# Kernel tuning notes

Measured on AMD Instinct MI355X. Metric: run time of the kernel, lower is better.

The kernel has to match this reference:

```python
import jax, jax.numpy as jnp
import numpy as np

N, E, F_IN, F_E, HID, HEADS = 20000, 320000, 256, 32, 128, 4
NEG_SLOPE = 0.2  # PyG GATConv default negative_slope


def _segment_softmax(logits, seg, num_segments):
    # logits: [E, H] softmax over edges sharing the same destination node
    m = jax.ops.segment_max(logits, seg, num_segments=num_segments)
    m = jnp.where(jnp.isfinite(m), m, 0.0)
    e = jnp.exp(logits - m[seg])
    s = jax.ops.segment_sum(e, seg, num_segments=num_segments)
    return e / s[seg]


def _gat_layer(x, edge_attr, src, dst, W, We, a_src, a_dst, a_edge, bias, num_nodes):
    H, C = a_src.shape
    h = (x @ W).reshape(-1, H, C)            # [N, H, C]
    he = (edge_attr @ We).reshape(-1, H, C)  # [E, H, C]
    alpha = (h * a_src).sum(-1)[src] + (h * a_dst).sum(-1)[dst] + (he * a_edge).sum(-1)
    alpha = jax.nn.leaky_relu(alpha, NEG_SLOPE)          # [E, H]
    alpha = _segment_softmax(alpha, dst, num_nodes)
    out = jax.ops.segment_sum(h[src] * alpha[..., None], dst, num_segments=num_nodes)
    return out.reshape(num_nodes, H * C) + bias


def setup_inputs() -> dict:
    key = jax.random.key(0)
    ks = jax.random.split(key, 20)
    s1 = 1.0 / np.sqrt(F_IN)
    s2 = 1.0 / np.sqrt(HID * HEADS)
    se = 1.0 / np.sqrt(F_E)
    sh = 1.0 / np.sqrt(HID)
    return {
        "x": jax.random.normal(ks[0], (N, F_IN), jnp.float32),
        "edge_index": jax.random.randint(ks[1], (2, E), 0, N),
        "edge_attr": jax.random.normal(ks[2], (E, F_E), jnp.float32),
        # GAT layer 1: in=F_IN, heads=HEADS, out=HID, concat=True
        "W1": jax.random.normal(ks[3], (F_IN, HEADS * HID), jnp.float32) * s1,
        "We1": jax.random.normal(ks[4], (F_E, HEADS * HID), jnp.float32) * se,
        "as1": jax.random.normal(ks[5], (HEADS, HID), jnp.float32) * sh,
        "ad1": jax.random.normal(ks[6], (HEADS, HID), jnp.float32) * sh,
        "ae1": jax.random.normal(ks[7], (HEADS, HID), jnp.float32) * sh,
        "b1": jnp.zeros((HEADS * HID,), jnp.float32),
        # GAT layer 2: in=HEADS*HID, heads=1, out=HID
        "W2": jax.random.normal(ks[8], (HEADS * HID, HID), jnp.float32) * s2,
        "We2": jax.random.normal(ks[9], (F_E, HID), jnp.float32) * se,
        "as2": jax.random.normal(ks[10], (1, HID), jnp.float32) * sh,
        "ad2": jax.random.normal(ks[11], (1, HID), jnp.float32) * sh,
        "ae2": jax.random.normal(ks[12], (1, HID), jnp.float32) * sh,
        "b2": jnp.zeros((HID,), jnp.float32),
        # projection head: Linear(HID,HID) -> PReLU -> Linear(HID,HID)
        "P1": jax.random.normal(ks[13], (HID, HID), jnp.float32) * sh,
        "pb1": jnp.zeros((HID,), jnp.float32),
        "prelu_a": jnp.float32(0.25),
        "P2": jax.random.normal(ks[14], (HID, HID), jnp.float32) * sh,
        "pb2": jnp.zeros((HID,), jnp.float32),
    }


def reference(x, edge_index, edge_attr, W1, We1, as1, ad1, ae1, b1,
              W2, We2, as2, ad2, ae2, b2, P1, pb1, prelu_a, P2, pb2):
    # eval mode: edge dropout / feature dropout are no-ops
    ei = jnp.concatenate([edge_index, edge_index[::-1]], axis=1)  # add reversed edges
    ea = jnp.concatenate([edge_attr, edge_attr], axis=0)
    src, dst = ei[0], ei[1]
    n = x.shape[0]
    h = jax.nn.elu(_gat_layer(x, ea, src, dst, W1, We1, as1, ad1, ae1, b1, n))
    h = jax.nn.elu(_gat_layer(h, ea, src, dst, W2, We2, as2, ad2, ae2, b2, n))
    z = h @ P1 + pb1
    z = jnp.where(z > 0, z, prelu_a * z)  # PReLU (single shared parameter)
    h_proj = z @ P2 + pb2
    g = jax.nn.sigmoid(h_proj.mean(axis=0))
    return h_proj, g
```

## Files before the change

### kernel.cpp

```cpp
#include <hip/hip_runtime.h>
#include <hip/hip_bf16.h>


#define NN    20000
#define EE    320000
#define E2    640000
#define FIN   256
#define FE    32
#define HIDD  128
#define NHEAD 4
#define HH    512
#define CAP   160
#define AW    132

typedef unsigned short ushort_t;
typedef short frag8 __attribute__((ext_vector_type(8)));
typedef float f32x4 __attribute__((ext_vector_type(4)));

__device__ inline ushort_t f2bf(float f){
  unsigned x = __float_as_uint(f);
  unsigned r = (x + 0x7fffu + ((x>>16)&1u)) >> 16;
  return (ushort_t)r;
}
__device__ inline float bf2f(ushort_t u){ return __uint_as_float(((unsigned)u)<<16); }
__device__ inline float lo_of(unsigned v){ return __uint_as_float(v<<16); }
__device__ inline float hi_of(unsigned v){ return __uint_as_float(v & 0xffff0000u); }

__global__ void prep(const int* __restrict__ ei, int* __restrict__ cnt,
                     const float* __restrict__ x, ushort_t* __restrict__ xb,
                     const float* __restrict__ W1, ushort_t* __restrict__ W1t,
                     const float* __restrict__ W2, ushort_t* __restrict__ W2t,
                     const float* __restrict__ P1, ushort_t* __restrict__ P1th, ushort_t* __restrict__ P1tl,
                     const float* __restrict__ P2, ushort_t* __restrict__ P2th, ushort_t* __restrict__ P2tl,
                     const float* __restrict__ We1, const float* __restrict__ ae1,
                     const float* __restrict__ We2, const float* __restrict__ ae2,
                     float* __restrict__ v1, float* __restrict__ v2){
  int b = blockIdx.x, tid = threadIdx.x;
  if(b < 2500){
    int e = b*256 + tid;
    int dst = (e < EE) ? ei[EE + e] : ei[e - EE];
    atomicAdd(&cnt[dst], 1);
  } else if(b < 7500){
    int i = (b-2500)*256 + tid;
    float4 v = ((const float4*)x)[i];
    ushort4 o; o.x=f2bf(v.x); o.y=f2bf(v.y); o.z=f2bf(v.z); o.w=f2bf(v.w);
    ((ushort4*)xb)[i] = o;
  } else if(b < 8012){
    int idx = (b-7500)*256 + tid;
    int k = idx>>9, n = idx&511;
    W1t[n*FIN + k] = f2bf(W1[idx]);
  } else if(b < 8268){
    int idx = (b-8012)*256 + tid;
    int k = idx>>7, n = idx&127;
    W2t[n*HH + k] = f2bf(W2[idx]);
  } else if(b < 8332){
    int idx = (b-8268)*256 + tid;
    int k = idx>>7, n = idx&127;
    float v = P1[idx];
    ushort_t h = f2bf(v);
    P1th[n*HIDD + k] = h;
    P1tl[n*HIDD + k] = f2bf(v - bf2f(h));
  } else if(b < 8396){
    int idx = (b-8332)*256 + tid;
    int k = idx>>7, n = idx&127;
    float v = P2[idx];
    ushort_t h = f2bf(v);
    P2th[n*HIDD + k] = h;
    P2tl[n*HIDD + k] = f2bf(v - bf2f(h));
  } else {
    if(tid < FE*NHEAD){
      int f = tid>>2, h = tid&3;
      float s = 0.f;
      for(int c=0;c<HIDD;c++) s += We1[f*HH + h*HIDD + c] * ae1[h*HIDD + c];
      v1[f*4+h] = s;
    } else if(tid < FE*NHEAD + FE){
      int f = tid - FE*NHEAD;
      float s = 0.f;
      for(int c=0;c<HIDD;c++) s += We2[f*HIDD + c] * ae2[c];
      v2[f] = s;
    }
  }
}

__global__ void scan_k(const int* __restrict__ cnt, int* __restrict__ rowptr){
  __shared__ int sums[1024];
  int tid = threadIdx.x;
  const int per = (NN + 1023)/1024;
  int base = tid*per;
  int s = 0;
  for(int i=0;i<per;i++){ int idx=base+i; if(idx<NN) s += cnt[idx]; }
  sums[tid] = s; __syncthreads();
  for(int off=1; off<1024; off<<=1){
    int v = (tid>=off)? sums[tid-off] : 0;
    __syncthreads();
    sums[tid] += v;
    __syncthreads();
  }
  int run = (tid==0)? 0 : sums[tid-1];
  for(int i=0;i<per;i++){
    int idx = base+i;
    if(idx<=NN) rowptr[idx] = run;
    if(idx<NN)  run += cnt[idx];
  }
}

__global__ __launch_bounds__(256) void csr_gemm1(
    const int* __restrict__ ei, const float* __restrict__ ea,
    const float* __restrict__ v1, const float* __restrict__ v2,
    const int* __restrict__ rowptr, int* __restrict__ fcnt,
    int* __restrict__ csrc, float* __restrict__ cae1, float* __restrict__ cae2,
    const ushort_t* __restrict__ A, const ushort_t* __restrict__ Bt,
    ushort_t* __restrict__ C, int M,
    const float* __restrict__ as1, const float* __restrict__ ad1,
    float* __restrict__ s1n, float* __restrict__ d1n){
  __shared__ ushort_t As[128*32];
  __shared__ ushort_t Bs[128*32];
  __shared__ float sred[2][128], dred[2][128];
  __shared__ float sv1[FE*NHEAD];
  __shared__ float sv2[FE];
  int tid = threadIdx.x;
  int b = blockIdx.x;
  if(b < 1250){
    if(tid < FE*NHEAD) sv1[tid] = v1[tid];
    if(tid < FE)       sv2[tid] = v2[tid];
    __syncthreads();
    int e = b*256 + tid;
    int a = ei[e], bb = ei[EE+e];
    const float4* er4 = (const float4*)(ea + (long)e*FE);
    float a0=0,a1=0,a2=0,a3=0,ab=0;
    #pragma unroll
    for(int f4=0; f4<FE/4; f4++){
      float4 t = er4[f4];
      float tv[4] = {t.x, t.y, t.z, t.w};
      #pragma unroll
      for(int c=0;c<4;c++){
        int f = f4*4+c;
        float t1 = tv[c];
        a0 += t1*sv1[f*4+0]; a1 += t1*sv1[f*4+1]; a2 += t1*sv1[f*4+2]; a3 += t1*sv1[f*4+3];
        ab += t1*sv2[f];
      }
    }
    float4 c4; c4.x=a0; c4.y=a1; c4.z=a2; c4.w=a3;
    int pos = rowptr[bb] + atomicAdd(&fcnt[bb], 1);
    csrc[pos] = a;
    *(float4*)(cae1 + (size_t)pos*4) = c4;
    cae2[pos] = ab;
    pos = rowptr[a] + atomicAdd(&fcnt[a], 1);
    csrc[pos] = bb;
    *(float4*)(cae1 + (size_t)pos*4) = c4;
    cae2[pos] = ab;
    return;
  }
  int g = b - 1250;
  int head = g & 3;
  int m0 = (g>>2)*128, n0 = head*128;
  int w = tid>>6, lane = tid&63;
  int qr = (w>>1)*64, qc = (w&1)*64;
  int lrow = lane&15, koff = (lane>>4)*8;
  f32x4 acc[4][4] = {};
  for(int k0=0; k0<FIN; k0+=32){
    #pragma unroll
    for(int rep=0;rep<2;rep++){
      int segid = tid + rep*256;
      int row = segid>>2, off = (segid&3)*8;
      int gr = m0 + row;
      int4 va = (gr<M) ? *(const int4*)(A + (long)gr*FIN + k0 + off) : int4{0,0,0,0};
      *(int4*)&As[row*32 + off] = va;
      int4 vb = *(const int4*)(Bt + (long)(n0+row)*FIN + k0 + off);
      *(int4*)&Bs[row*32 + off] = vb;
    }
    __syncthreads();
    frag8 af[4], bfr[4];
    #pragma unroll
    for(int i=0;i<4;i++) af[i]  = *(const frag8*)&As[(qr + i*16 + lrow)*32 + koff];
    #pragma unroll
    for(int j=0;j<4;j++) bfr[j] = *(const frag8*)&Bs[(qc + j*16 + lrow)*32 + koff];
    #pragma unroll
    for(int i=0;i<4;i++)
      #pragma unroll
      for(int j=0;j<4;j++)
        acc[i][j] = __builtin_amdgcn_mfma_f32_16x16x32_bf16(af[i], bfr[j], acc[i][j], 0,0,0);
    __syncthreads();
  }
  #pragma unroll
  for(int i=0;i<4;i++)
    #pragma unroll
    for(int j=0;j<4;j++)
      #pragma unroll
      for(int r=0;r<4;r++){
        int row = m0 + qr + i*16 + (lane>>4)*4 + r;
        int col = n0 + qc + j*16 + (lane&15);
        if(row<M) C[(long)row*HH + col] = f2bf(acc[i][j][r]);
      }
  float a_s[4], a_d[4];
  #pragma unroll
  for(int j=0;j<4;j++){
    a_s[j] = as1[head*HIDD + qc + j*16 + (lane&15)];
    a_d[j] = ad1[head*HIDD + qc + j*16 + (lane&15)];
  }
  #pragma unroll
  for(int i=0;i<4;i++)
    #pragma unroll
    for(int r=0;r<4;r++){
      float sp = acc[i][0][r]*a_s[0] + acc[i][1][r]*a_s[1] + acc[i][2][r]*a_s[2] + acc[i][3][r]*a_s[3];
      float dp = acc[i][0][r]*a_d[0] + acc[i][1][r]*a_d[1] + acc[i][2][r]*a_d[2] + acc[i][3][r]*a_d[3];
      #pragma unroll
      for(int o=1;o<=8;o<<=1){ sp += __shfl_xor(sp,o,64); dp += __shfl_xor(dp,o,64); }
      if((lane&15)==0){
        int rl = qr + i*16 + (lane>>4)*4 + r;
        sred[w&1][rl] = sp;
        dred[w&1][rl] = dp;
      }
    }
  __syncthreads();
  if(tid < 128){
    int gr = m0 + tid;
    if(gr < M){
      s1n[gr*4 + head] = sred[0][tid] + sred[1][tid];
      d1n[gr*4 + head] = dred[0][tid] + dred[1][tid];
    }
  }
}

__global__ __launch_bounds__(256) void gemm64_attn(const ushort_t* __restrict__ A, const ushort_t* __restrict__ Bt,
                                                   ushort_t* __restrict__ C, int M,
                                                   const float* __restrict__ as2, const float* __restrict__ ad2,
                                                   float* __restrict__ s2n, float* __restrict__ d2n){
  __shared__ ushort_t As[64*32];
  __shared__ ushort_t Bs[128*32];
  __shared__ float sred[4][64], dred[4][64];
  int tid = threadIdx.x;
  int m0 = blockIdx.y*64;
  int w = tid>>6, lane = tid&63;
  int qc = w*32;
  int lrow = lane&15, koff = (lane>>4)*8;
  f32x4 acc[4][2] = {};
  for(int k0=0; k0<HH; k0+=32){
    {
      int row = tid>>2, off = (tid&3)*8;
      int gr = m0 + row;
      int4 va = (gr<M) ? *(const int4*)(A + (long)gr*HH + k0 + off) : int4{0,0,0,0};
      *(int4*)&As[row*32 + off] = va;
    }
    #pragma unroll
    for(int rep=0;rep<2;rep++){
      int segid = tid + rep*256;
      int row = segid>>2, off = (segid&3)*8;
      int4 vb = *(const int4*)(Bt + (long)row*HH + k0 + off);
      *(int4*)&Bs[row*32 + off] = vb;
    }
    __syncthreads();
    frag8 af[4], bfr[2];
    #pragma unroll
    for(int i=0;i<4;i++) af[i]  = *(const frag8*)&As[(i*16 + lrow)*32 + koff];
    #pragma unroll
    for(int j=0;j<2;j++) bfr[j] = *(const frag8*)&Bs[(qc + j*16 + lrow)*32 + koff];
    #pragma unroll
    for(int i=0;i<4;i++)
      #pragma unroll
      for(int j=0;j<2;j++)
        acc[i][j] = __builtin_amdgcn_mfma_f32_16x16x32_bf16(af[i], bfr[j], acc[i][j], 0,0,0);
    __syncthreads();
  }
  #pragma unroll
  for(int i=0;i<4;i++)
    #pragma unroll
    for(int j=0;j<2;j++)
      #pragma unroll
      for(int r=0;r<4;r++){
        int row = m0 + i*16 + (lane>>4)*4 + r;
        int col = qc + j*16 + (lane&15);
        if(row<M) C[(long)row*HIDD + col] = f2bf(acc[i][j][r]);
      }
  float a_s[2], a_d[2];
  #pragma unroll
  for(int j=0;j<2;j++){
    a_s[j] = as2[qc + j*16 + (lane&15)];
    a_d[j] = ad2[qc + j*16 + (lane&15)];
  }
  #pragma unroll
  for(int i=0;i<4;i++)
    #pragma unroll
    for(int r=0;r<4;r++){
      float sp = acc[i][0][r]*a_s[0] + acc[i][1][r]*a_s[1];
      float dp = acc[i][0][r]*a_d[0] + acc[i][1][r]*a_d[1];
      #pragma unroll
      for(int o=1;o<=8;o<<=1){ sp += __shfl_xor(sp,o,64); dp += __shfl_xor(dp,o,64); }
      if((lane&15)==0){
        int rl = i*16 + (lane>>4)*4 + r;
        sred[w][rl] = sp;
        dred[w][rl] = dp;
      }
    }
  __syncthreads();
  if(tid < 64){
    int gr = m0 + tid;
    if(gr < M){
      s2n[gr] = sred[0][tid]+sred[1][tid]+sred[2][tid]+sred[3][tid];
      d2n[gr] = dred[0][tid]+dred[1][tid]+dred[2][tid]+dred[3][tid];
    }
  }
}

__global__ __launch_bounds__(256) void agg1(const ushort_t* __restrict__ h1b, const int* __restrict__ rowptr,
                     const int* __restrict__ csrc,
                     const float* __restrict__ s1n, const float* __restrict__ d1n,
                     const float* __restrict__ cae1,
                     const float* __restrict__ b1, ushort_t* __restrict__ out1b){
  __shared__ float stlog[4][CAP*4];
  __shared__ int   sidx[4][CAP];
  int tid = threadIdx.x;
  int wv = tid>>6, lane = tid&63;
  int n = blockIdx.x*4 + wv;
  int beg = rowptr[n], end = rowptr[n+1];
  int deg = end - beg;
  int h12 = lane&3;
  float dh = d1n[n*4 + h12];
  float m = -1e30f, ss = 0.f;
  for(int base=beg; base<end; base+=16){
    int e = base + (lane>>2);
    if(e<end){
      int s = csrc[e];
      float t = s1n[s*4 + h12] + dh + cae1[e*4 + h12];
      t = t>0.f? t : 0.2f*t;
      int j = e - beg;
      if(j < CAP){
        stlog[wv][j*4 + h12] = t;
        if(h12==0) sidx[wv][j] = s;
      }
      float nm = fmaxf(m, t);
      ss = ss*__expf(m-nm) + __expf(t-nm);
      m = nm;
    }
  }
  #pragma unroll
  for(int o=4;o<=32;o<<=1){
    float mo = __shfl_xor(m, o, 64), so = __shfl_xor(ss, o, 64);
    float nm = fmaxf(m, mo);
    ss = ss*__expf(m-nm) + so*__expf(mo-nm);
    m = nm;
  }
  float inv = ss>0.f ? 1.f/ss : 0.f;
  int hq = lane>>4;
  float mq   = __shfl(m,   hq, 64);
  float invq = __shfl(inv, hq, 64);
  float dhq  = d1n[n*4 + hq];
  int capn = deg < CAP ? deg : CAP;
  float acc[8] = {};
  int j = 0;
  for(; j+3<capn; j+=4){
    int s0 = sidx[wv][j], s1 = sidx[wv][j+1], s2 = sidx[wv][j+2], s3 = sidx[wv][j+3];
    float w0 = __expf(stlog[wv][(j  )*4 + hq] - mq)*invq;
    float w1 = __expf(stlog[wv][(j+1)*4 + hq] - mq)*invq;
    float w2 = __expf(stlog[wv][(j+2)*4 + hq] - mq)*invq;
    float w3 = __expf(stlog[wv][(j+3)*4 + hq] - mq)*invq;
    uint4 v0 = *(const uint4*)(h1b + (long)s0*HH + lane*8);
    uint4 v1 = *(const uint4*)(h1b + (long)s1*HH + lane*8);
    uint4 v2 = *(const uint4*)(h1b + (long)s2*HH + lane*8);
    uint4 v3 = *(const uint4*)(h1b + (long)s3*HH + lane*8);
    acc[0] += w0*lo_of(v0.x) + w1*lo_of(v1.x) + w2*lo_of(v2.x) + w3*lo_of(v3.x);
    acc[1] += w0*hi_of(v0.x) + w1*hi_of(v1.x) + w2*hi_of(v2.x) + w3*hi_of(v3.x);
    acc[2] += w0*lo_of(v0.y) + w1*lo_of(v1.y) + w2*lo_of(v2.y) + w3*lo_of(v3.y);
    acc[3] += w0*hi_of(v0.y) + w1*hi_of(v1.y) + w2*hi_of(v2.y) + w3*hi_of(v3.y);
    acc[4] += w0*lo_of(v0.z) + w1*lo_of(v1.z) + w2*lo_of(v2.z) + w3*lo_of(v3.z);
    acc[5] += w0*hi_of(v0.z) + w1*hi_of(v1.z) + w2*hi_of(v2.z) + w3*hi_of(v3.z);
    acc[6] += w0*lo_of(v0.w) + w1*lo_of(v1.w) + w2*lo_of(v2.w) + w3*lo_of(v3.w);
    acc[7] += w0*hi_of(v0.w) + w1*hi_of(v1.w) + w2*hi_of(v2.w) + w3*hi_of(v3.w);
  }
  for(; j<capn; j++){
    int s0 = sidx[wv][j];
    float w0 = __expf(stlog[wv][j*4 + hq] - mq)*invq;
    uint4 v0 = *(const uint4*)(h1b + (long)s0*HH + lane*8);
    acc[0] += w0*lo_of(v0.x); acc[1] += w0*hi_of(v0.x);
    acc[2] += w0*lo_of(v0.y); acc[3] += w0*hi_of(v0.y);
    acc[4] += w0*lo_of(v0.z); acc[5] += w0*hi_of(v0.z);
    acc[6] += w0*lo_of(v0.w); acc[7] += w0*hi_of(v0.w);
  }
  for(; j<deg; j++){
    int e = beg + j;
    int s0 = csrc[e];
    float t = s1n[s0*4 + hq] + dhq + cae1[e*4 + hq];
    t = t>0.f? t : 0.2f*t;
    float w0 = __expf(t - mq)*invq;
    uint4 v0 = *(const uint4*)(h1b + (long)s0*HH + lane*8);
    acc[0] += w0*lo_of(v0.x); acc[1] += w0*hi_of(v0.x);
    acc[2] += w0*lo_of(v0.y); acc[3] += w0*hi_of(v0.y);
    acc[4] += w0*lo_of(v0.z); acc[5] += w0*hi_of(v0.z);
    acc[6] += w0*lo_of(v0.w); acc[7] += w0*hi_of(v0.w);
  }
  float4 bl = ((const float4*)b1)[lane*2];
  float4 bh = ((const float4*)b1)[lane*2+1];
  float bb[8] = {bl.x,bl.y,bl.z,bl.w,bh.x,bh.y,bh.z,bh.w};
  ushort_t o8[8];
  #pragma unroll
  for(int c=0;c<8;c++){
    float o = acc[c] + bb[c];
    o8[c] = f2bf(o>0.f? o : __expf(o)-1.f);
  }
  uint4 pk;
  pk.x = (unsigned)o8[0] | ((unsigned)o8[1]<<16);
  pk.y = (unsigned)o8[2] | ((unsigned)o8[3]<<16);
  pk.z = (unsigned)o8[4] | ((unsigned)o8[5]<<16);
  pk.w = (unsigned)o8[6] | ((unsigned)o8[7]<<16);
  *(uint4*)(out1b + (long)n*HH + lane*8) = pk;
}

__global__ __launch_bounds__(256) void agg2(const ushort_t* __restrict__ h2b, const int* __restrict__ rowptr,
                     const int* __restrict__ csrc,
                     const float* __restrict__ s2n, const float* __restrict__ d2n,
                     const float* __restrict__ cae2,
                     const float* __restrict__ b2, float* __restrict__ out2){
  __shared__ float stl[4][CAP];
  __shared__ int   sid[4][CAP];
  int tid = threadIdx.x;
  int wv = tid>>6, lane = tid&63;
  int n = blockIdx.x*4 + wv;
  int beg = rowptr[n], end = rowptr[n+1];
  int deg = end - beg;
  float dn = d2n[n];
  float m = -1e30f, ss = 0.f;
  for(int e=beg+lane; e<end; e+=64){
    int s = csrc[e];
    float t = s2n[s] + dn + cae2[e];
    t = t>0.f? t : 0.2f*t;
    int j = e - beg;
    if(j < CAP){ stl[wv][j] = t; sid[wv][j] = s; }
    float nm = fmaxf(m, t);
    ss = ss*__expf(m-nm) + __expf(t-nm);
    m = nm;
  }
  #pragma unroll
  for(int o=1;o<=32;o<<=1){
    float mo = __shfl_xor(m, o, 64), so = __shfl_xor(ss, o, 64);
    float nm = fmaxf(m, mo);
    ss = ss*__expf(m-nm) + so*__expf(mo-nm);
    m = nm;
  }
  float inv = ss>0.f ? 1.f/ss : 0.f;
  int capn = deg < CAP ? deg : CAP;
  float a0=0.f, a1=0.f;
  int j = 0;
  for(; j+3<capn; j+=4){
    int s0 = sid[wv][j], s1 = sid[wv][j+1], s2 = sid[wv][j+2], s3 = sid[wv][j+3];
    float w0 = __expf(stl[wv][j]  -m)*inv;
    float w1 = __expf(stl[wv][j+1]-m)*inv;
    float w2 = __expf(stl[wv][j+2]-m)*inv;
    float w3 = __expf(stl[wv][j+3]-m)*inv;
    unsigned v0 = *(const unsigned*)(h2b + (long)s0*HIDD + 2*lane);
    unsigned v1 = *(const unsigned*)(h2b + (long)s1*HIDD + 2*lane);
    unsigned v2 = *(const unsigned*)(h2b + (long)s2*HIDD + 2*lane);
    unsigned v3 = *(const unsigned*)(h2b + (long)s3*HIDD + 2*lane);
    a0 += w0*lo_of(v0) + w1*lo_of(v1) + w2*lo_of(v2) + w3*lo_of(v3);
    a1 += w0*hi_of(v0) + w1*hi_of(v1) + w2*hi_of(v2) + w3*hi_of(v3);
  }
  for(; j<capn; j++){
    float w0 = __expf(stl[wv][j]-m)*inv;
    unsigned v0 = *(const unsigned*)(h2b + (long)sid[wv][j]*HIDD + 2*lane);
    a0 += w0*lo_of(v0); a1 += w0*hi_of(v0);
  }
  for(; j<deg; j++){
    int e = beg + j;
    int s0 = csrc[e];
    float t = s2n[s0] + dn + cae2[e];
    t = t>0.f? t : 0.2f*t;
    float w0 = __expf(t-m)*inv;
    unsigned v0 = *(const unsigned*)(h2b + (long)s0*HIDD + 2*lane);
    a0 += w0*lo_of(v0); a1 += w0*hi_of(v0);
  }
  float o0 = a0 + b2[2*lane];
  float o1 = a1 + b2[2*lane+1];
  float2 pk;
  pk.x = o0>0.f? o0 : __expf(o0)-1.f;
  pk.y = o1>0.f? o1 : __expf(o1)-1.f;
  *(float2*)(out2 + (long)n*HIDD + 2*lane) = pk;
}

__global__ __launch_bounds__(256) void proj_fused(const float* __restrict__ A,
    const ushort_t* __restrict__ P1th, const ushort_t* __restrict__ P1tl,
    const ushort_t* __restrict__ P2th, const ushort_t* __restrict__ P2tl,
    const float* __restrict__ pb1, const float* __restrict__ pra,
    const float* __restrict__ pb2, float* __restrict__ OUT, int M,
    float* __restrict__ gbuf){
  __shared__ ushort_t Ah[64*AW], Al[64*AW];
  __shared__ ushort_t Bh[128*32], Bl[128*32];
  int tid = threadIdx.x;
  int m0 = blockIdx.x*64;
  int w = tid>>6, lane = tid&63;
  int qc = w*32;
  int lrow = lane&15, koff2 = (lane>>4)*8;
  f32x4 acc[4][2] = {};
  {
    int row = tid>>2, cb = (tid&3)*8;
    int gr = m0 + row;
    for(int c0=0;c0<HIDD;c0+=32){
      float4 u0{0,0,0,0}, u1{0,0,0,0};
      if(gr<M){
        u0 = *(const float4*)(A + (long)gr*HIDD + c0 + cb);
        u1 = *(const float4*)(A + (long)gr*HIDD + c0 + cb + 4);
      }
      float vv[8] = {u0.x,u0.y,u0.z,u0.w,u1.x,u1.y,u1.z,u1.w};
      unsigned ph[4], pl[4];
      #pragma unroll
      for(int c=0;c<4;c++){
        ushort_t h0 = f2bf(vv[2*c]),   l0 = f2bf(vv[2*c]   - bf2f(h0));
        ushort_t h1 = f2bf(vv[2*c+1]), l1 = f2bf(vv[2*c+1] - bf2f(h1));
        ph[c] = (unsigned)h0 | ((unsigned)h1<<16);
        pl[c] = (unsigned)l0 | ((unsigned)l1<<16);
      }
      *(uint4*)&Ah[row*AW + c0 + cb] = *(uint4*)ph;
      *(uint4*)&Al[row*AW + c0 + cb] = *(uint4*)pl;
    }
  }
  __syncthreads();
  for(int k0=0;k0<HIDD;k0+=32){
    #pragma unroll
    for(int rep=0;rep<2;rep++){
      int segid = tid + rep*256;
      int row = segid>>2, off = (segid&3)*8;
      *(int4*)&Bh[row*32 + off] = *(const int4*)(P1th + (long)row*HIDD + k0 + off);
      *(int4*)&Bl[row*32 + off] = *(const int4*)(P1tl + (long)row*HIDD + k0 + off);
    }
    __syncthreads();
    frag8 afh[4], afl[4], bfh[2], bfl[2];
    #pragma unroll
    for(int i=0;i<4;i++){
      afh[i] = *(const frag8*)&Ah[(i*16 + lrow)*AW + k0 + koff2];
      afl[i] = *(const frag8*)&Al[(i*16 + lrow)*AW + k0 + koff2];
    }
    #pragma unroll
    for(int j=0;j<2;j++){
      bfh[j] = *(const frag8*)&Bh[(qc + j*16 + lrow)*32 + koff2];
      bfl[j] = *(const frag8*)&Bl[(qc + j*16 + lrow)*32 + koff2];
    }
    #pragma unroll
    for(int i=0;i<4;i++)
      #pragma unroll
      for(int j=0;j<2;j++){
        acc[i][j] = __builtin_amdgcn_mfma_f32_16x16x32_bf16(afh[i], bfh[j], acc[i][j], 0,0,0);
        acc[i][j] = __builtin_amdgcn_mfma_f32_16x16x32_bf16(afh[i], bfl[j], acc[i][j], 0,0,0);
        acc[i][j] = __builtin_amdgcn_mfma_f32_16x16x32_bf16(afl[i], bfh[j], acc[i][j], 0,0,0);
      }
    __syncthreads();
  }
  float ap = pra[0];
  #pragma unroll
  for(int i=0;i<4;i++)
    #pragma unroll
    for(int j=0;j<2;j++)
      #pragma unroll
      for(int r=0;r<4;r++){
        int row = i*16 + (lane>>4)*4 + r;
        int col = qc + j*16 + (lane&15);
        float v = acc[i][j][r] + pb1[col];
        v = v>0.f? v : ap*v;
        ushort_t h = f2bf(v);
        Ah[row*AW + col] = h;
        Al[row*AW + col] = f2bf(v - bf2f(h));
        acc[i][j][r] = 0.f;
      }
  __syncthreads();
  for(int k0=0;k0<HIDD;k0+=32){
    #pragma unroll
    for(int rep=0;rep<2;rep++){
      int segid = tid + rep*256;
      int row = segid>>2, off = (segid&3)*8;
      *(int4*)&Bh[row*32 + off] = *(const int4*)(P2th + (long)row*HIDD + k0 + off);
      *(int4*)&Bl[row*32 + off] = *(const int4*)(P2tl + (long)row*HIDD + k0 + off);
    }
    __syncthreads();
    frag8 afh[4], afl[4], bfh[2], bfl[2];
    #pragma unroll
    for(int i=0;i<4;i++){
      afh[i] = *(const frag8*)&Ah[(i*16 + lrow)*AW + k0 + koff2];
      afl[i] = *(const frag8*)&Al[(i*16 + lrow)*AW + k0 + koff2];
    }
    #pragma unroll
    for(int j=0;j<2;j++){
      bfh[j] = *(const frag8*)&Bh[(qc + j*16 + lrow)*32 + koff2];
      bfl[j] = *(const frag8*)&Bl[(qc + j*16 + lrow)*32 + koff2];
    }
    #pragma unroll
    for(int i=0;i<4;i++)
      #pragma unroll
      for(int j=0;j<2;j++){
        acc[i][j] = __builtin_amdgcn_mfma_f32_16x16x32_bf16(afh[i], bfh[j], acc[i][j], 0,0,0);
        acc[i][j] = __builtin_amdgcn_mfma_f32_16x16x32_bf16(afh[i], bfl[j], acc[i][j], 0,0,0);
        acc[i][j] = __builtin_amdgcn_mfma_f32_16x16x32_bf16(afl[i], bfh[j], acc[i][j], 0,0,0);
      }
    __syncthreads();
  }
  float cs[2] = {0.f, 0.f};
  #pragma unroll
  for(int i=0;i<4;i++)
    #pragma unroll
    for(int j=0;j<2;j++)
      #pragma unroll
      for(int r=0;r<4;r++){
        int rowg = m0 + i*16 + (lane>>4)*4 + r;
        int col = qc + j*16 + (lane&15);
        if(rowg<M){
          float v = acc[i][j][r] + pb2[col];
          OUT[(long)rowg*HIDD + col] = v;
          cs[j] += v;
        }
      }
  #pragma unroll
  for(int j=0;j<2;j++){
    cs[j] += __shfl_xor(cs[j],16,64);
    cs[j] += __shfl_xor(cs[j],32,64);
    if((lane>>4)==0) atomicAdd(&gbuf[qc + j*16 + (lane&15)], cs[j]);
  }
}

__global__ void sigmoid_g(const float* __restrict__ gbuf, float* __restrict__ gout){
  int c = threadIdx.x;
  float m = gbuf[c] * (1.0f/NN);
  gout[c] = 1.f/(1.f+__expf(-m));
}


extern "C" void kernel_launch(void* const* d_in, const int* in_sizes, int n_in,
                              void* d_out, int out_size, void* d_ws, size_t ws_size,
                              hipStream_t stream){
  const float* x    = (const float*)d_in[0];
  const int*   ei   = (const int*)  d_in[1];
  const float* ea   = (const float*)d_in[2];
  const float* W1   = (const float*)d_in[3];
  const float* We1  = (const float*)d_in[4];
  const float* as1  = (const float*)d_in[5];
  const float* ad1  = (const float*)d_in[6];
  const float* ae1  = (const float*)d_in[7];
  const float* b1   = (const float*)d_in[8];
  const float* W2   = (const float*)d_in[9];
  const float* We2  = (const float*)d_in[10];
  const float* as2  = (const float*)d_in[11];
  const float* ad2  = (const float*)d_in[12];
  const float* ae2  = (const float*)d_in[13];
  const float* b2   = (const float*)d_in[14];
  const float* P1   = (const float*)d_in[15];
  const float* pb1  = (const float*)d_in[16];
  const float* pra  = (const float*)d_in[17];
  const float* P2   = (const float*)d_in[18];
  const float* pb2  = (const float*)d_in[19];
  float* out = (float*)d_out;

  char* wsp = (char*)d_ws;
  size_t off = 0;
  auto alloc = [&](size_t bytes)->char*{
    char* p = wsp + off;
    off += (bytes + 255) & ~(size_t)255;
    return p;
  };
  ushort_t* h1b  = (ushort_t*)alloc(sizeof(ushort_t)*(size_t)NN*HH);
  ushort_t* out1b= (ushort_t*)alloc(sizeof(ushort_t)*(size_t)NN*HH);
  ushort_t* h2b  = (ushort_t*)alloc(sizeof(ushort_t)*(size_t)NN*HIDD);
  float*    out2 = (float*)  alloc(sizeof(float)*(size_t)NN*HIDD);
  ushort_t* xb   = (ushort_t*)alloc(sizeof(ushort_t)*(size_t)NN*FIN);
  ushort_t* W1t  = (ushort_t*)alloc(sizeof(ushort_t)*(size_t)HH*FIN);
  ushort_t* W2t  = (ushort_t*)alloc(sizeof(ushort_t)*(size_t)HIDD*HH);
  ushort_t* P1th = (ushort_t*)alloc(sizeof(ushort_t)*(size_t)HIDD*HIDD);
  ushort_t* P1tl = (ushort_t*)alloc(sizeof(ushort_t)*(size_t)HIDD*HIDD);
  ushort_t* P2th = (ushort_t*)alloc(sizeof(ushort_t)*(size_t)HIDD*HIDD);
  ushort_t* P2tl = (ushort_t*)alloc(sizeof(ushort_t)*(size_t)HIDD*HIDD);
  float* s1n   = (float*)alloc(sizeof(float)*NN*NHEAD);
  float* d1n   = (float*)alloc(sizeof(float)*NN*NHEAD);
  float* s2n   = (float*)alloc(sizeof(float)*NN);
  float* d2n   = (float*)alloc(sizeof(float)*NN);
  float* v1    = (float*)alloc(sizeof(float)*FE*NHEAD);
  float* v2    = (float*)alloc(sizeof(float)*FE);
  float* cae1  = (float*)alloc(sizeof(float)*(size_t)E2*NHEAD);
  float* cae2  = (float*)alloc(sizeof(float)*(size_t)E2);
  int*   rowptr= (int*)  alloc(sizeof(int)*(NN+1));
  int*   csrc  = (int*)  alloc(sizeof(int)*(size_t)E2);
  int*   cnt   = (int*)  alloc(sizeof(int)*NN);
  int*   fcnt  = (int*)  alloc(sizeof(int)*NN);
  float* gbuf  = (float*)alloc(sizeof(float)*HIDD);

  hipMemsetAsync(cnt, 0, 80128 + 80128 + 512, stream);

  prep     <<<8397, 256, 0, stream>>>(ei, cnt, x, xb, W1, W1t, W2, W2t,
                                      P1, P1th, P1tl, P2, P2th, P2tl,
                                      We1, ae1, We2, ae2, v1, v2);
  scan_k   <<<1, 1024, 0, stream>>>(cnt, rowptr);
  csr_gemm1<<<1250 + 628, 256, 0, stream>>>(ei, ea, v1, v2, rowptr, fcnt, csrc, cae1, cae2,
                                            xb, W1t, h1b, NN, as1, ad1, s1n, d1n);
  agg1     <<<NN/4, 256, 0, stream>>>(h1b, rowptr, csrc, s1n, d1n, cae1, b1, out1b);
  gemm64_attn<<<dim3(1, (NN+63)/64), 256, 0, stream>>>(out1b, W2t, h2b, NN, as2, ad2, s2n, d2n);
  agg2     <<<NN/4, 256, 0, stream>>>(h2b, rowptr, csrc, s2n, d2n, cae2, b2, out2);
  proj_fused<<<(NN+63)/64, 256, 0, stream>>>(out2, P1th, P1tl, P2th, P2tl,
                                             pb1, pra, pb2, out, NN, gbuf);
  sigmoid_g<<<1, 128, 0, stream>>>(gbuf, out + (size_t)NN*HIDD);
}
```

Before: 394.8 us.

## Split agg1 nodes across two waves, precompute softmax weights, vectorize scan

Result: faster. 373.4 us (-5.4%).

```diff
diff --git a/kernel.cpp b/kernel.cpp
--- a/kernel.cpp
+++ b/kernel.cpp
@@ -85,23 +85,38 @@
 __global__ void scan_k(const int* __restrict__ cnt, int* __restrict__ rowptr){
   __shared__ int sums[1024];
   int tid = threadIdx.x;
-  const int per = (NN + 1023)/1024;
+  const int per = 20;
   int base = tid*per;
+  int v[20];
+  if(base + per <= NN){
+    #pragma unroll
+    for(int q=0;q<5;q++) *(int4*)&v[q*4] = *(const int4*)&cnt[base + q*4];
+  } else {
+    for(int i=0;i<per;i++) v[i] = (base+i<NN)? cnt[base+i] : 0;
+  }
   int s = 0;
-  for(int i=0;i<per;i++){ int idx=base+i; if(idx<NN) s += cnt[idx]; }
+  #pragma unroll
+  for(int i=0;i<per;i++) s += v[i];
   sums[tid] = s; __syncthreads();
   for(int off=1; off<1024; off<<=1){
-    int v = (tid>=off)? sums[tid-off] : 0;
-    __syncthreads();
-    sums[tid] += v;
+    int t = (tid>=off)? sums[tid-off] : 0;
+    __syncthreads();
+    sums[tid] += t;
     __syncthreads();
   }
   int run = (tid==0)? 0 : sums[tid-1];
-  for(int i=0;i<per;i++){
-    int idx = base+i;
-    if(idx<=NN) rowptr[idx] = run;
-    if(idx<NN)  run += cnt[idx];
-  }
+  int rp[20];
+  #pragma unroll
+  for(int i=0;i<per;i++){ rp[i] = run; run += v[i]; }
+  if(base + per <= NN){
+    #pragma unroll
+    for(int q=0;q<5;q++) *(int4*)&rowptr[base + q*4] = *(const int4*)&rp[q*4];
+  } else {
+    for(int i=0;i<per;i++) if(base+i<=NN) rowptr[base+i] = rp[i];
+  }
+  if(base == NN) rowptr[NN] = rp[0];
+  if(tid == 1023 && base + per == NN) rowptr[NN] = run;
+  if(tid == 1000) rowptr[NN] = rp[0];
 }
 
 __global__ __launch_bounds__(256) void csr_gemm1(
@@ -307,17 +322,20 @@
                      const float* __restrict__ s1n, const float* __restrict__ d1n,
                      const float* __restrict__ cae1,
                      const float* __restrict__ b1, ushort_t* __restrict__ out1b){
-  __shared__ float stlog[4][CAP*4];
-  __shared__ int   sidx[4][CAP];
+  __shared__ float stw[2][CAP*4];
+  __shared__ int   sidx[2][CAP];
+  __shared__ float pm[2][2][4], ps[2][2][4];
   int tid = threadIdx.x;
-  int wv = tid>>6, lane = tid&63;
-  int n = blockIdx.x*4 + wv;
+  int nodeLoc = tid>>7;
+  int wv2 = (tid>>6)&1;
+  int lane = tid&63;
+  int n = blockIdx.x*2 + nodeLoc;
   int beg = rowptr[n], end = rowptr[n+1];
   int deg = end - beg;
   int h12 = lane&3;
   float dh = d1n[n*4 + h12];
   float m = -1e30f, ss = 0.f;
-  for(int base=beg; base<end; base+=16){
+  for(int base=beg + wv2*16; base<end; base+=32){
     int e = base + (lane>>2);
     if(e<end){
       int s = csrc[e];
@@ -325,8 +343,8 @@
       t = t>0.f? t : 0.2f*t;
       int j = e - beg;
       if(j < CAP){
-        stlog[wv][j*4 + h12] = t;
-        if(h12==0) sidx[wv][j] = s;
+        stw[nodeLoc][j*4 + h12] = t;
+        if(h12==0) sidx[nodeLoc][j] = s;
       }
       float nm = fmaxf(m, t);
       ss = ss*__expf(m-nm) + __expf(t-nm);
@@ -340,69 +358,69 @@
     ss = ss*__expf(m-nm) + so*__expf(mo-nm);
     m = nm;
   }
-  float inv = ss>0.f ? 1.f/ss : 0.f;
-  int hq = lane>>4;
-  float mq   = __shfl(m,   hq, 64);
-  float invq = __shfl(inv, hq, 64);
-  float dhq  = d1n[n*4 + hq];
+  if(lane<4){ pm[nodeLoc][wv2][lane] = m; ps[nodeLoc][wv2][lane] = ss; }
+  __syncthreads();
+  float m4[4], i4[4];
+  #pragma unroll
+  for(int h=0;h<4;h++){
+    float mA = pm[nodeLoc][0][h], mB = pm[nodeLoc][1][h];
+    float sA = ps[nodeLoc][0][h], sB = ps[nodeLoc][1][h];
+    float mf = fmaxf(mA, mB);
+    float sf = sA*__expf(mA-mf) + sB*__expf(mB-mf);
+    m4[h] = mf; i4[h] = sf>0.f ? 1.f/sf : 0.f;
+  }
   int capn = deg < CAP ? deg : CAP;
-  float acc[8] = {};
+  int tln = tid & 127;
+  float mh = m4[h12], ih = i4[h12];
+  for(int f=tln; f<capn*4; f+=128) stw[nodeLoc][f] = __expf(stw[nodeLoc][f]-mh)*ih;
+  __syncthreads();
+  int hq = wv2*2 + (lane>>5);
+  long cOff = (long)(wv2*256 + lane*4);
+  float acc0=0.f, acc1=0.f, acc2=0.f, acc3=0.f;
   int j = 0;
   for(; j+3<capn; j+=4){
-    int s0 = sidx[wv][j], s1 = sidx[wv][j+1], s2 = sidx[wv][j+2], s3 = sidx[wv][j+3];
-    float w0 = __expf(stlog[wv][(j  )*4 + hq] - mq)*invq;
-    float w1 = __expf(stlog[wv][(j+1)*4 + hq] - mq)*invq;
-    float w2 = __expf(stlog[wv][(j+2)*4 + hq] - mq)*invq;
-    float w3 = __expf(stlog[wv][(j+3)*4 + hq] - mq)*invq;
-    uint4 v0 = *(const uint4*)(h1b + (long)s0*HH + lane*8);
-    uint4 v1 = *(const uint4*)(h1b + (long)s1*HH + lane*8);
-    uint4 v2 = *(const uint4*)(h1b + (long)s2*HH + lane*8);
-    uint4 v3 = *(const uint4*)(h1b + (long)s3*HH + lane*8);
-    acc[0] += w0*lo_of(v0.x) + w1*lo_of(v1.x) + w2*lo_of(v2.x) + w3*lo_of(v3.x);
-    acc[1] += w0*hi_of(v0.x) + w1*hi_of(v1.x) + w2*hi_of(v2.x) + w3*hi_of(v3.x);
-    acc[2] += w0*lo_of(v0.y) + w1*lo_of(v1.y) + w2*lo_of(v2.y) + w3*lo_of(v3.y);
-    acc[3] += w0*hi_of(v0.y) + w1*hi_of(v1.y) + w2*hi_of(v2.y) + w3*hi_of(v3.y);
-    acc[4] += w0*lo_of(v0.z) + w1*lo_of(v1.z) + w2*lo_of(v2.z) + w3*lo_of(v3.z);
-    acc[5] += w0*hi_of(v0.z) + w1*hi_of(v1.z) + w2*hi_of(v2.z) + w3*hi_of(v3.z);
-    acc[6] += w0*lo_of(v0.w) + w1*lo_of(v1.w) + w2*lo_of(v2.w) + w3*lo_of(v3.w);
-    acc[7] += w0*hi_of(v0.w) + w1*hi_of(v1.w) + w2*hi_of(v2.w) + w3*hi_of(v3.w);
+    int s0 = sidx[nodeLoc][j],   s1 = sidx[nodeLoc][j+1];
+    int s2 = sidx[nodeLoc][j+2], s3 = sidx[nodeLoc][j+3];
+    float w0 = stw[nodeLoc][(j  )*4 + hq];
+    float w1 = stw[nodeLoc][(j+1)*4 + hq];
+    float w2 = stw[nodeLoc][(j+2)*4 + hq];
+    float w3 = stw[nodeLoc][(j+3)*4 + hq];
+    uint2 v0 = *(const uint2*)(h1b + (long)s0*HH + cOff);
+    uint2 v1 = *(const uint2*)(h1b + (long)s1*HH + cOff);
+    uint2 v2 = *(const uint2*)(h1b + (long)s2*HH + cOff);
+    uint2 v3 = *(const uint2*)(h1b + (long)s3*HH + cOff);
+    acc0 += w0*lo_of(v0.x) + w1*lo_of(v1.x) + w2*lo_of(v2.x) + w3*lo_of(v3.x);
+    acc1 += w0*hi_of(v0.x) + w1*hi_of(v1.x) + w2*hi_of(v2.x) + w3*hi_of(v3.x);
+    acc2 += w0*lo_of(v0.y) + w1*lo_of(v1.y) + w2*lo_of(v2.y) + w3*lo_of(v3.y);
+    acc3 += w0*hi_of(v0.y) + w1*hi_of(v1.y) + w2*hi_of(v2.y) + w3*hi_of(v3.y);
   }
   for(; j<capn; j++){
-    int s0 = sidx[wv][j];
-    float w0 = __expf(stlog[wv][j*4 + hq] - mq)*invq;
-    uint4 v0 = *(const uint4*)(h1b + (long)s0*HH + lane*8);
-    acc[0] += w0*lo_of(v0.x); acc[1] += w0*hi_of(v0.x);
-    acc[2] += w0*lo_of(v0.y); acc[3] += w0*hi_of(v0.y);
-    acc[4] += w0*lo_of(v0.z); acc[5] += w0*hi_of(v0.z);
-    acc[6] += w0*lo_of(v0.w); acc[7] += w0*hi_of(v0.w);
+    int s0 = sidx[nodeLoc][j];
+    float w0 = stw[nodeLoc][j*4 + hq];
+    uint2 v0 = *(const uint2*)(h1b + (long)s0*HH + cOff);
+    acc0 += w0*lo_of(v0.x); acc1 += w0*hi_of(v0.x);
+    acc2 += w0*lo_of(v0.y); acc3 += w0*hi_of(v0.y);
   }
   for(; j<deg; j++){
     int e = beg + j;
     int s0 = csrc[e];
-    float t = s1n[s0*4 + hq] + dhq + cae1[e*4 + hq];
+    float t = s1n[s0*4 + hq] + d1n[n*4 + hq] + cae1[e*4 + hq];
     t = t>0.f? t : 0.2f*t;
-    float w0 = __expf(t - mq)*invq;
-    uint4 v0 = *(const uint4*)(h1b + (long)s0*HH + lane*8);
-    acc[0] += w0*lo_of(v0.x); acc[1] += w0*hi_of(v0.x);
-    acc[2] += w0*lo_of(v0.y); acc[3] += w0*hi_of(v0.y);
-    acc[4] += w0*lo_of(v0.z); acc[5] += w0*hi_of(v0.z);
-    acc[6] += w0*lo_of(v0.w); acc[7] += w0*hi_of(v0.w);
-  }
-  float4 bl = ((const float4*)b1)[lane*2];
-  float4 bh = ((const float4*)b1)[lane*2+1];
-  float bb[8] = {bl.x,bl.y,bl.z,bl.w,bh.x,bh.y,bh.z,bh.w};
-  ushort_t o8[8];
-  #pragma unroll
-  for(int c=0;c<8;c++){
-    float o = acc[c] + bb[c];
-    o8[c] = f2bf(o>0.f? o : __expf(o)-1.f);
-  }
-  uint4 pk;
-  pk.x = (unsigned)o8[0] | ((unsigned)o8[1]<<16);
-  pk.y = (unsigned)o8[2] | ((unsigned)o8[3]<<16);
-  pk.z = (unsigned)o8[4] | ((unsigned)o8[5]<<16);
-  pk.w = (unsigned)o8[6] | ((unsigned)o8[7]<<16);
-  *(uint4*)(out1b + (long)n*HH + lane*8) = pk;
+    float w0 = __expf(t - m4[hq])*i4[hq];
+    uint2 v0 = *(const uint2*)(h1b + (long)s0*HH + cOff);
+    acc0 += w0*lo_of(v0.x); acc1 += w0*hi_of(v0.x);
+    acc2 += w0*lo_of(v0.y); acc3 += w0*hi_of(v0.y);
+  }
+  float4 bb = *(const float4*)(b1 + cOff);
+  float o0 = acc0 + bb.x, o1 = acc1 + bb.y, o2 = acc2 + bb.z, o3 = acc3 + bb.w;
+  o0 = o0>0.f? o0 : __expf(o0)-1.f;
+  o1 = o1>0.f? o1 : __expf(o1)-1.f;
+  o2 = o2>0.f? o2 : __expf(o2)-1.f;
+  o3 = o3>0.f? o3 : __expf(o3)-1.f;
+  uint2 pk;
+  pk.x = (unsigned)f2bf(o0) | ((unsigned)f2bf(o1)<<16);
+  pk.y = (unsigned)f2bf(o2) | ((unsigned)f2bf(o3)<<16);
+  *(uint2*)(out1b + (long)n*HH + cOff) = pk;
 }
 
 __global__ __launch_bounds__(256) void agg2(const ushort_t* __restrict__ h2b, const int* __restrict__ rowptr,
@@ -438,14 +456,12 @@
   }
   float inv = ss>0.f ? 1.f/ss : 0.f;
   int capn = deg < CAP ? deg : CAP;
+  for(int j=lane; j<capn; j+=64) stl[wv][j] = __expf(stl[wv][j]-m)*inv;
   float a0=0.f, a1=0.f;
   int j = 0;
   for(; j+3<capn; j+=4){
     int s0 = sid[wv][j], s1 = sid[wv][j+1], s2 = sid[wv][j+2], s3 = sid[wv][j+3];
-    float w0 = __expf(stl[wv][j]  -m)*inv;
-    float w1 = __expf(stl[wv][j+1]-m)*inv;
-    float w2 = __expf(stl[wv][j+2]-m)*inv;
-    float w3 = __expf(stl[wv][j+3]-m)*inv;
+    float w0 = stl[wv][j], w1 = stl[wv][j+1], w2 = stl[wv][j+2], w3 = stl[wv][j+3];
     unsigned v0 = *(const unsigned*)(h2b + (long)s0*HIDD + 2*lane);
     unsigned v1 = *(const unsigned*)(h2b + (long)s1*HIDD + 2*lane);
     unsigned v2 = *(const unsigned*)(h2b + (long)s2*HIDD + 2*lane);
@@ -454,7 +470,7 @@
     a1 += w0*hi_of(v0) + w1*hi_of(v1) + w2*hi_of(v2) + w3*hi_of(v3);
   }
   for(; j<capn; j++){
-    float w0 = __expf(stl[wv][j]-m)*inv;
+    float w0 = stl[wv][j];
     unsigned v0 = *(const unsigned*)(h2b + (long)sid[wv][j]*HIDD + 2*lane);
     a0 += w0*lo_of(v0); a1 += w0*hi_of(v0);
   }
@@ -684,7 +700,7 @@
   scan_k   <<<1, 1024, 0, stream>>>(cnt, rowptr);
   csr_gemm1<<<1250 + 628, 256, 0, stream>>>(ei, ea, v1, v2, rowptr, fcnt, csrc, cae1, cae2,
                                             xb, W1t, h1b, NN, as1, ad1, s1n, d1n);
-  agg1     <<<NN/4, 256, 0, stream>>>(h1b, rowptr, csrc, s1n, d1n, cae1, b1, out1b);
+  agg1     <<<NN/2, 256, 0, stream>>>(h1b, rowptr, csrc, s1n, d1n, cae1, b1, out1b);
   gemm64_attn<<<dim3(1, (NN+63)/64), 256, 0, stream>>>(out1b, W2t, h2b, NN, as2, ad2, s2n, d2n);
   agg2     <<<NN/4, 256, 0, stream>>>(h2b, rowptr, csrc, s2n, d2n, cae2, b2, out2);
   proj_fused<<<(NN+63)/64, 256, 0, stream>>>(out2, P1th, P1tl, P2th, P2tl,
```
